# Optimization experiments

Measured on AMD Instinct MI355X. Metric: run time of the kernel, lower is better.

The kernel has to match this reference:

```python
import jax, jax.numpy as jnp
import numpy as np

KNN = 11  # self.knn in VoronoiBaseNN


def setup_inputs() -> dict:
    key = jax.random.key(0)
    k1, k2 = jax.random.split(key)
    points = jax.random.normal(k1, (2, 50000, 3), dtype=jnp.float32)   # GT surface samples
    spoints = jax.random.normal(k2, (2, 4000, 3), dtype=jnp.float32)   # Voronoi generators
    return {"points": points, "spoints": spoints}


def reference(points, spoints):
    # Pairwise squared distances: [B, N, M]
    d2 = ((points[:, :, None, :] - spoints[:, None, :, :]) ** 2).sum(-1)
    # KNN smallest, sorted ascending (torch.topk(largest=False, sorted=True))
    _, idx = jax.lax.top_k(-d2, KNN)            # idx: [B, N, KNN]
    # Gather the KNN generator coordinates: [B, N, KNN, 3]
    gathered = jax.vmap(lambda sp, i: sp[i])(spoints, idx)
    inside = gathered[:, :, 0, :]               # closest cell center [B, N, 3]
    point_to_center = points - inside           # [B, N, 3]
    # Voronoi edge vectors to the other KNN-1 neighbors: [B, N, KNN-1, 3]
    voronoi_edge = gathered[:, :, 1:, :] - inside[:, :, None, :]
    edge_l = jnp.sqrt((voronoi_edge ** 2).sum(-1))                      # [B, N, KNN-1]
    vector_length = (point_to_center[:, :, None, :] * voronoi_edge).sum(-1) / edge_l
    sq_dist = (vector_length - edge_l / 2.0) ** 2
    return sq_dist.min(-1)                      # [B, N]
```

## Files before the change

kernel.cpp:

```cpp
#include <hip/hip_runtime.h>
#include <math.h>

#define NPTS  50000
#define NSP   4000
#define NGRP  1000
#define NW    4
#define QW    (NGRP / NW)
#define QC    (NSP  / NW)
#define KNN   11
#define BIG   3.4e38f
#define SEGCAP 256
#define SEGPAD 8
#define SEGSTR (SEGCAP + SEGPAD)
#define GRIDC 32
#define NKEY  65536

#define MED3(a,b,c) __builtin_amdgcn_fmed3f((a),(b),(c))

__device__ unsigned g_hist[NKEY];
__device__ float4   g_sorted[2 * NPTS];

static __device__ __forceinline__ unsigned spread5(unsigned v) {
    return (v & 1u) | ((v & 2u) << 2) | ((v & 4u) << 4) |
           ((v & 8u) << 6) | ((v & 16u) << 8);
}

static __device__ __forceinline__ unsigned cell_key(int b, float x, float y, float z) {
    int gx = (int)floorf((x + 4.0f) * 4.0f);
    int gy = (int)floorf((y + 4.0f) * 4.0f);
    int gz = (int)floorf((z + 4.0f) * 4.0f);
    gx = min(max(gx, 0), GRIDC - 1);
    gy = min(max(gy, 0), GRIDC - 1);
    gz = min(max(gz, 0), GRIDC - 1);
    unsigned m = spread5((unsigned)gx) | (spread5((unsigned)gy) << 1) |
                 (spread5((unsigned)gz) << 2);
    return ((unsigned)b << 15) | m;
}

__global__ void k_zero() {
    int t = blockIdx.x * 256 + threadIdx.x;
    if (t < NKEY) g_hist[t] = 0u;
}

__global__ void k_hist(const float* __restrict__ pts) {
    int n = blockIdx.x * 256 + threadIdx.x;
    if (n >= 2 * NPTS) return;
    const float* p = pts + (size_t)n * 3;
    int b = (n >= NPTS) ? 1 : 0;
    atomicAdd(&g_hist[cell_key(b, p[0], p[1], p[2])], 1u);
}

__global__ void k_scan() {
    __shared__ unsigned part[1024];
    const int t = threadIdx.x;
    const unsigned base = (unsigned)blockIdx.x * 32768u + (unsigned)t * 32u;
    unsigned s = 0;
#pragma unroll
    for (int j = 0; j < 32; ++j) s += g_hist[base + j];
    part[t] = s;
    __syncthreads();
    for (int off = 1; off < 1024; off <<= 1) {
        unsigned v = (t >= off) ? part[t - off] : 0u;
        __syncthreads();
        part[t] += v;
        __syncthreads();
    }
    unsigned run = (unsigned)blockIdx.x * (unsigned)NPTS + part[t] - s;
#pragma unroll
    for (int j = 0; j < 32; ++j) {
        unsigned h = g_hist[base + j];
        g_hist[base + j] = run;
        run += h;
    }
}

__global__ void k_scatter(const float* __restrict__ pts) {
    int n = blockIdx.x * 256 + threadIdx.x;
    if (n >= 2 * NPTS) return;
    const float* p = pts + (size_t)n * 3;
    int b = (n >= NPTS) ? 1 : 0;
    float x = p[0], y = p[1], z = p[2];
    unsigned dst = atomicAdd(&g_hist[cell_key(b, x, y, z)], 1u);
    if (dst < 2u * NPTS)
        g_sorted[dst] = make_float4(x, y, z, __uint_as_float((unsigned)(n - b * NPTS)));
}

static __device__ __forceinline__ float wred_min(float v) {
#pragma unroll
    for (int off = 32; off > 0; off >>= 1) v = fminf(v, __shfl_xor(v, off, 64));
    return v;
}
static __device__ __forceinline__ float wred_max(float v) {
#pragma unroll
    for (int off = 32; off > 0; off >>= 1) v = fmaxf(v, __shfl_xor(v, off, 64));
    return v;
}

__global__ __launch_bounds__(256, 4) void voronoi_kernel(
    const float* __restrict__ spts,
    float* __restrict__ out)
{
    __shared__ float4 sl[NW * SEGSTR];
    __shared__ float  lds_d[NW][64][13];
    __shared__ int    lds_i[NW][64];
    __shared__ float  lds_b[NW][64];
    __shared__ float  lds_m[NW];

    const int b    = blockIdx.y;
    const int lane = threadIdx.x & 63;
    const int wq   = threadIdx.x >> 6;
    int pi = blockIdx.x * 64 + lane;
    const bool valid = (pi < NPTS);
    if (!valid) pi = NPTS - 1;

    const float4 P = g_sorted[(size_t)b * NPTS + pi];
    const float px = P.x, py = P.y, pz = P.z;
    const unsigned orig = __float_as_uint(P.w);

    const float mnx = wred_min(px), mxx = wred_max(px);
    const float mny = wred_min(py), mxy = wred_max(py);
    const float mnz = wred_min(pz), mxz = wred_max(pz);
    const float ccx = 0.5f * (mnx + mxx);
    const float ccy = 0.5f * (mny + mxy);
    const float ccz = 0.5f * (mnz + mxz);
    const float R = sqrtf(wred_max(
        fmaf(px - ccx, px - ccx, fmaf(py - ccy, py - ccy, (pz - ccz) * (pz - ccz)))));

    const float4* __restrict__ spq = (const float4*)(spts + (size_t)b * NSP * 3);
    const int g0 = wq * QW, g1 = g0 + QW;

    float myMin = BIG;
    for (int k0 = g0; k0 < g1; k0 += 64) {
        const int g  = k0 + lane;
        const int gc = (g < g1) ? g : (g1 - 1);
        const float4 q0 = spq[3 * gc + 0];
        const float4 q1 = spq[3 * gc + 1];
        const float4 q2 = spq[3 * gc + 2];
        float dx = q0.x - ccx, dy = q0.y - ccy, dz = q0.z - ccz;
        float md = fmaf(dx, dx, fmaf(dy, dy, dz * dz));
        dx = q0.w - ccx; dy = q1.x - ccy; dz = q1.y - ccz;
        md = fminf(md, fmaf(dx, dx, fmaf(dy, dy, dz * dz)));
        dx = q1.z - ccx; dy = q1.w - ccy; dz = q2.x - ccz;
        md = fminf(md, fmaf(dx, dx, fmaf(dy, dy, dz * dz)));
        dx = q2.y - ccx; dy = q2.z - ccy; dz = q2.w - ccz;
        md = fminf(md, fmaf(dx, dx, fmaf(dy, dy, dz * dz)));
        if (g < g1) myMin = fminf(myMin, md);
    }
    float vv = myMin, m11 = 0.0f;
#pragma unroll
    for (int t = 0; t < KNN; ++t) {
        m11 = wred_min(vv);
        vv = (vv == m11) ? BIG : vv;
    }
    if (lane == 0) lds_m[wq] = m11;
    __syncthreads();
    const float m11g = fminf(fminf(lds_m[0], lds_m[1]), fminf(lds_m[2], lds_m[3]));
    const float Trad = sqrtf(m11g) + R;
    const float T = Trad * Trad * 1.0004f + 1e-12f;

    const int segbase = wq * SEGSTR;
    unsigned cnt = 0;
    {
        for (int k0 = g0; k0 < g1; k0 += 64) {
            const int g  = k0 + lane;
            const int gc = (g < g1) ? g : (g1 - 1);
            const bool in = (g < g1);
            const float4 q0 = spq[3 * gc + 0];
            const float4 q1 = spq[3 * gc + 1];
            const float4 q2 = spq[3 * gc + 2];
#define ADM(sx, sy, sz) \
            (fmaf(MED3((sx), mnx, mxx) - (sx), MED3((sx), mnx, mxx) - (sx), \
             fmaf(MED3((sy), mny, mxy) - (sy), MED3((sy), mny, mxy) - (sy), \
                  (MED3((sz), mnz, mxz) - (sz)) * (MED3((sz), mnz, mxz) - (sz)))) <= T)
#define PUSH(sx, sy, sz, ok, idx) { \
            const unsigned long long msk = __ballot(ok); \
            const unsigned pos = cnt + \
                __builtin_amdgcn_mbcnt_hi((unsigned)(msk >> 32), \
                    __builtin_amdgcn_mbcnt_lo((unsigned)msk, 0u)); \
            if ((ok) && pos < SEGCAP) \
                sl[segbase + pos] = make_float4((sx), (sy), (sz), \
                                                __uint_as_float((unsigned)(idx))); \
            cnt += (unsigned)__popcll(msk); }
            const bool a0 = in && ADM(q0.x, q0.y, q0.z);
            const bool a1 = in && ADM(q0.w, q1.x, q1.y);
            const bool a2 = in && ADM(q1.z, q1.w, q2.x);
            const bool a3 = in && ADM(q2.y, q2.z, q2.w);
            PUSH(q0.x, q0.y, q0.z, a0, 4 * gc + 0);
            PUSH(q0.w, q1.x, q1.y, a1, 4 * gc + 1);
            PUSH(q1.z, q1.w, q2.x, a2, 4 * gc + 2);
            PUSH(q2.y, q2.z, q2.w, a3, 4 * gc + 3);
        }
        if (lane < SEGPAD) {
            const unsigned cb = (cnt <= SEGCAP) ? cnt : SEGCAP;
            sl[segbase + cb + lane] =
                make_float4(1e18f, 1e18f, 1e18f, __uint_as_float(0x7fffffffu));
        }
    }
    const bool myfast = (cnt <= SEGCAP);

    float d0 = BIG, d1 = BIG, d2 = BIG, d3 = BIG, d4 = BIG, d5 = BIG,
          d6 = BIG, d7 = BIG, d8 = BIG, d9 = BIG, d10 = BIG;
    int i0 = 0x7fffffff;

#define CHAIN(nd, jj) { \
        if (__ballot((nd) < d10)) { \
            d10 = MED3(d9, d10, (nd)); \
            d9  = MED3(d8, d9,  (nd)); \
            d8  = MED3(d7, d8,  (nd)); \
            d7  = MED3(d6, d7,  (nd)); \
            d6  = MED3(d5, d6,  (nd)); \
            d5  = MED3(d4, d5,  (nd)); \
            d4  = MED3(d3, d4,  (nd)); \
            d3  = MED3(d2, d3,  (nd)); \
            d2  = MED3(d1, d2,  (nd)); \
            d1  = MED3(d0, d1,  (nd)); \
            i0  = ((nd) < d0) ? (jj) : i0; \
            d0  = fminf(d0, (nd)); \
        } }
#define CANDA(c) { \
        const float dx = px - (c).x, dy = py - (c).y, dz = pz - (c).z; \
        const float nd = fmaf(dx, dx, fmaf(dy, dy, dz * dz)); \
        const int jj = (int)__float_as_uint((c).w); \
        CHAIN(nd, jj); }

    const float* sp = spts + (size_t)b * NSP * 3 + wq * (QC * 3);
    const int jb = wq * QC;

    if (myfast) {
        if (cnt > 0) {
            float4 c0 = sl[segbase + 0], c1 = sl[segbase + 1],
                   c2 = sl[segbase + 2], c3 = sl[segbase + 3];
            for (unsigned k = 0; k < cnt; k += 4) {
                const float4 n0 = sl[segbase + k + 4];
                const float4 n1 = sl[segbase + k + 5];
                const float4 n2 = sl[segbase + k + 6];
                const float4 n3 = sl[segbase + k + 7];
                CANDA(c0); CANDA(c1); CANDA(c2); CANDA(c3);
                c0 = n0; c1 = n1; c2 = n2; c3 = n3;
            }
        }
    } else {
        for (int j = 0; j < QC; j += 4) {
            const float4 q0 = *(const float4*)(sp + j * 3);
            const float4 q1 = *(const float4*)(sp + j * 3 + 4);
            const float4 q2 = *(const float4*)(sp + j * 3 + 8);
            { const float dx = px - q0.x, dy = py - q0.y, dz = pz - q0.z;
              const float nd = fmaf(dx, dx, fmaf(dy, dy, dz * dz)); CHAIN(nd, jb + j); }
            { const float dx = px - q0.w, dy = py - q1.x, dz = pz - q1.y;
              const float nd = fmaf(dx, dx, fmaf(dy, dy, dz * dz)); CHAIN(nd, jb + j + 1); }
            { const float dx = px - q1.z, dy = py - q1.w, dz = pz - q2.x;
              const float nd = fmaf(dx, dx, fmaf(dy, dy, dz * dz)); CHAIN(nd, jb + j + 2); }
            { const float dx = px - q2.y, dy = py - q2.z, dz = pz - q2.w;
              const float nd = fmaf(dx, dx, fmaf(dy, dy, dz * dz)); CHAIN(nd, jb + j + 3); }
        }
    }

    lds_d[wq][lane][0]  = d0;  lds_d[wq][lane][1]  = d1;
    lds_d[wq][lane][2]  = d2;  lds_d[wq][lane][3]  = d3;
    lds_d[wq][lane][4]  = d4;  lds_d[wq][lane][5]  = d5;
    lds_d[wq][lane][6]  = d6;  lds_d[wq][lane][7]  = d7;
    lds_d[wq][lane][8]  = d8;  lds_d[wq][lane][9]  = d9;
    lds_d[wq][lane][10] = d10;
    lds_i[wq][lane] = i0;
    __syncthreads();

    float gb = BIG; int gi = 0x7fffffff;
#pragma unroll
    for (int q = 0; q < NW; ++q) {
        const float dq = lds_d[q][lane][0];
        const int   iq = lds_i[q][lane];
        const bool take = (dq < gb) || (dq == gb && iq < gi);
        gb = take ? dq : gb;
        gi = take ? iq : gi;
    }
#define INS(v) { \
        d10 = MED3(d9, d10, (v)); \
        d9  = MED3(d8, d9,  (v)); \
        d8  = MED3(d7, d8,  (v)); \
        d7  = MED3(d6, d7,  (v)); \
        d6  = MED3(d5, d6,  (v)); \
        d5  = MED3(d4, d5,  (v)); \
        d4  = MED3(d3, d4,  (v)); \
        d3  = MED3(d2, d3,  (v)); \
        d2  = MED3(d1, d2,  (v)); \
        d1  = MED3(d0, d1,  (v)); \
        d0  = fminf(d0, (v)); }
#pragma unroll
    for (int q = 0; q < NW; ++q) {
        if (q == wq) continue;
#pragma unroll
        for (int k = 0; k < 11; ++k) INS(lds_d[q][lane][k]);
    }
    const float d10g = d10;
    const int   i0g  = gi;

    const float* ip = spts + (size_t)b * NSP * 3 + (size_t)(unsigned)i0g * 3;
    const float ix = ip[0], iy = ip[1], iz = ip[2];
    const float vx = px - ix, vy = py - iy, vz = pz - iz;
    float best = BIG;

#define EDGE(sx, sy, sz, adm) { \
        if (__ballot(adm)) { \
            const float ex = (sx) - ix, ey = (sy) - iy, ez = (sz) - iz; \
            const float ee = fmaf(ex, ex, fmaf(ey, ey, ez * ez)); \
            const float dt = fmaf(vx, ex, fmaf(vy, ey, vz * ez)); \
            const float u  = fmaf(-0.5f, ee, dt); \
            const float t2 = u * u * __builtin_amdgcn_rcpf(ee); \
            best = (adm) ? fminf(best, t2) : best; \
        } }
#define CANDB(c) { \
        const float dx = px - (c).x, dy = py - (c).y, dz = pz - (c).z; \
        const float nd = fmaf(dx, dx, fmaf(dy, dy, dz * dz)); \
        const int jj = (int)__float_as_uint((c).w); \
        const bool adm = (nd <= d10g) && (jj != i0g); \
        EDGE((c).x, (c).y, (c).z, adm); }

    if (myfast) {
        if (cnt > 0) {
            float4 c0 = sl[segbase + 0], c1 = sl[segbase + 1],
                   c2 = sl[segbase + 2], c3 = sl[segbase + 3];
            for (unsigned k = 0; k < cnt; k += 4) {
                const float4 n0 = sl[segbase + k + 4];
                const float4 n1 = sl[segbase + k + 5];
                const float4 n2 = sl[segbase + k + 6];
                const float4 n3 = sl[segbase + k + 7];
                CANDB(c0); CANDB(c1); CANDB(c2); CANDB(c3);
                c0 = n0; c1 = n1; c2 = n2; c3 = n3;
            }
        }
    } else {
        for (int j = 0; j < QC; j += 4) {
            const float4 q0 = *(const float4*)(sp + j * 3);
            const float4 q1 = *(const float4*)(sp + j * 3 + 4);
            const float4 q2 = *(const float4*)(sp + j * 3 + 8);
            { const float dx = px - q0.x, dy = py - q0.y, dz = pz - q0.z;
              const float nd = fmaf(dx, dx, fmaf(dy, dy, dz * dz));
              const bool adm = (nd <= d10g) && ((jb + j) != i0g);
              EDGE(q0.x, q0.y, q0.z, adm); }
            { const float dx = px - q0.w, dy = py - q1.x, dz = pz - q1.y;
              const float nd = fmaf(dx, dx, fmaf(dy, dy, dz * dz));
              const bool adm = (nd <= d10g) && ((jb + j + 1) != i0g);
              EDGE(q0.w, q1.x, q1.y, adm); }
            { const float dx = px - q1.z, dy = py - q1.w, dz = pz - q2.x;
              const float nd = fmaf(dx, dx, fmaf(dy, dy, dz * dz));
              const bool adm = (nd <= d10g) && ((jb + j + 2) != i0g);
              EDGE(q1.z, q1.w, q2.x, adm); }
            { const float dx = px - q2.y, dy = py - q2.z, dz = pz - q2.w;
              const float nd = fmaf(dx, dx, fmaf(dy, dy, dz * dz));
              const bool adm = (nd <= d10g) && ((jb + j + 3) != i0g);
              EDGE(q2.y, q2.z, q2.w, adm); }
        }
    }

    lds_b[wq][lane] = best;
    __syncthreads();
    if (wq == 0) {
        float m = fminf(fminf(lds_b[0][lane], lds_b[1][lane]),
                        fminf(lds_b[2][lane], lds_b[3][lane]));
        if (valid) out[(size_t)b * NPTS + orig] = m;
    }
}

extern "C" void kernel_launch(void* const* d_in, const int* in_sizes, int n_in,
                              void* d_out, int out_size, void* d_ws, size_t ws_size,
                              hipStream_t stream) {
    (void)in_sizes; (void)n_in; (void)d_ws; (void)ws_size; (void)out_size;
    const float* pts  = (const float*)d_in[0];
    const float* spts = (const float*)d_in[1];
    float* out = (float*)d_out;

    k_zero   <<<dim3(NKEY / 256),            dim3(256),  0, stream>>>();
    k_hist   <<<dim3((2 * NPTS + 255)/256),  dim3(256),  0, stream>>>(pts);
    k_scan   <<<dim3(2),                     dim3(1024), 0, stream>>>();
    k_scatter<<<dim3((2 * NPTS + 255)/256),  dim3(256),  0, stream>>>(pts);
    voronoi_kernel<<<dim3((NPTS + 63)/64, 2), dim3(256), 0, stream>>>(spts, out);
}
```

Measured before the change: 306.0 us.

## Split wave into four 16-lane sub-boxes for tighter candidate culling

Instead of one bounding box and radius per 64-point wave, the kernel computes four bounding boxes over 16-lane subgroups, each with its own kth-nearest threshold. A generator is admitted if it falls within the threshold of any sub-box, which is meant to shrink the candidate list scanned in the KNN and edge passes. The brute-force overflow fallback is replaced by chunked re-collection into a larger LDS segment (capacity doubled), with the edge pass redoing collection when overflow occurred. The cost is four times the threshold arithmetic and more LDS, with occupancy lowered from 4 to 3 blocks per SIMD in the launch bounds.

```diff
diff --git a/kernel.cpp b/kernel.cpp
--- a/kernel.cpp
+++ b/kernel.cpp
@@ -6,10 +6,9 @@
 #define NGRP  1000
 #define NW    4
 #define QW    (NGRP / NW)
-#define QC    (NSP  / NW)
 #define KNN   11
 #define BIG   3.4e38f
-#define SEGCAP 256
+#define SEGCAP 512
 #define SEGPAD 8
 #define SEGSTR (SEGCAP + SEGPAD)
 #define GRIDC 32
@@ -90,13 +89,18 @@
     for (int off = 32; off > 0; off >>= 1) v = fminf(v, __shfl_xor(v, off, 64));
     return v;
 }
-static __device__ __forceinline__ float wred_max(float v) {
-#pragma unroll
-    for (int off = 32; off > 0; off >>= 1) v = fmaxf(v, __shfl_xor(v, off, 64));
+static __device__ __forceinline__ float sred_min16(float v) {
+#pragma unroll
+    for (int off = 8; off > 0; off >>= 1) v = fminf(v, __shfl_xor(v, off, 64));
     return v;
 }
-
-__global__ __launch_bounds__(256, 4) void voronoi_kernel(
+static __device__ __forceinline__ float sred_max16(float v) {
+#pragma unroll
+    for (int off = 8; off > 0; off >>= 1) v = fmaxf(v, __shfl_xor(v, off, 64));
+    return v;
+}
+
+__global__ __launch_bounds__(256, 3) void voronoi_kernel(
     const float* __restrict__ spts,
     float* __restrict__ out)
 {
@@ -104,7 +108,7 @@
     __shared__ float  lds_d[NW][64][13];
     __shared__ int    lds_i[NW][64];
     __shared__ float  lds_b[NW][64];
-    __shared__ float  lds_m[NW];
+    __shared__ float  lds_m[NW][4];
 
     const int b    = blockIdx.y;
     const int lane = threadIdx.x & 63;
@@ -117,86 +121,131 @@
     const float px = P.x, py = P.y, pz = P.z;
     const unsigned orig = __float_as_uint(P.w);
 
-    const float mnx = wred_min(px), mxx = wred_max(px);
-    const float mny = wred_min(py), mxy = wred_max(py);
-    const float mnz = wred_min(pz), mxz = wred_max(pz);
-    const float ccx = 0.5f * (mnx + mxx);
-    const float ccy = 0.5f * (mny + mxy);
-    const float ccz = 0.5f * (mnz + mxz);
-    const float R = sqrtf(wred_max(
-        fmaf(px - ccx, px - ccx, fmaf(py - ccy, py - ccy, (pz - ccz) * (pz - ccz)))));
+    const float smnx = sred_min16(px), smxx = sred_max16(px);
+    const float smny = sred_min16(py), smxy = sred_max16(py);
+    const float smnz = sred_min16(pz), smxz = sred_max16(pz);
+    const float scx = 0.5f * (smnx + smxx);
+    const float scy = 0.5f * (smny + smxy);
+    const float scz = 0.5f * (smnz + smxz);
+    const float sR = sqrtf(sred_max16(
+        fmaf(px - scx, px - scx, fmaf(py - scy, py - scy, (pz - scz) * (pz - scz)))));
+
+#define BC(v, j) __shfl((v), (j) * 16, 64)
+    const float b0nx = BC(smnx,0), b0xx = BC(smxx,0), b0ny = BC(smny,0),
+                b0xy = BC(smxy,0), b0nz = BC(smnz,0), b0xz = BC(smxz,0),
+                c0x = BC(scx,0), c0y = BC(scy,0), c0z = BC(scz,0), R0 = BC(sR,0);
+    const float b1nx = BC(smnx,1), b1xx = BC(smxx,1), b1ny = BC(smny,1),
+                b1xy = BC(smxy,1), b1nz = BC(smnz,1), b1xz = BC(smxz,1),
+                c1x = BC(scx,1), c1y = BC(scy,1), c1z = BC(scz,1), R1 = BC(sR,1);
+    const float b2nx = BC(smnx,2), b2xx = BC(smxx,2), b2ny = BC(smny,2),
+                b2xy = BC(smxy,2), b2nz = BC(smnz,2), b2xz = BC(smxz,2),
+                c2x = BC(scx,2), c2y = BC(scy,2), c2z = BC(scz,2), R2 = BC(sR,2);
+    const float b3nx = BC(smnx,3), b3xx = BC(smxx,3), b3ny = BC(smny,3),
+                b3xy = BC(smxy,3), b3nz = BC(smnz,3), b3xz = BC(smxz,3),
+                c3x = BC(scx,3), c3y = BC(scy,3), c3z = BC(scz,3), R3 = BC(sR,3);
 
     const float4* __restrict__ spq = (const float4*)(spts + (size_t)b * NSP * 3);
     const int g0 = wq * QW, g1 = g0 + QW;
 
-    float myMin = BIG;
+    float v0 = BIG, v1 = BIG, v2 = BIG, v3 = BIG;
     for (int k0 = g0; k0 < g1; k0 += 64) {
         const int g  = k0 + lane;
         const int gc = (g < g1) ? g : (g1 - 1);
         const float4 q0 = spq[3 * gc + 0];
         const float4 q1 = spq[3 * gc + 1];
         const float4 q2 = spq[3 * gc + 2];
-        float dx = q0.x - ccx, dy = q0.y - ccy, dz = q0.z - ccz;
-        float md = fmaf(dx, dx, fmaf(dy, dy, dz * dz));
-        dx = q0.w - ccx; dy = q1.x - ccy; dz = q1.y - ccz;
-        md = fminf(md, fmaf(dx, dx, fmaf(dy, dy, dz * dz)));
-        dx = q1.z - ccx; dy = q1.w - ccy; dz = q2.x - ccz;
-        md = fminf(md, fmaf(dx, dx, fmaf(dy, dy, dz * dz)));
-        dx = q2.y - ccx; dy = q2.z - ccy; dz = q2.w - ccz;
-        md = fminf(md, fmaf(dx, dx, fmaf(dy, dy, dz * dz)));
-        if (g < g1) myMin = fminf(myMin, md);
-    }
-    float vv = myMin, m11 = 0.0f;
+        float t0 = BIG, t1 = BIG, t2 = BIG, t3 = BIG;
+#define DACC(sx, sy, sz) { \
+        float dx, dy, dz; \
+        dx=(sx)-c0x; dy=(sy)-c0y; dz=(sz)-c0z; t0=fminf(t0, fmaf(dx,dx,fmaf(dy,dy,dz*dz))); \
+        dx=(sx)-c1x; dy=(sy)-c1y; dz=(sz)-c1z; t1=fminf(t1, fmaf(dx,dx,fmaf(dy,dy,dz*dz))); \
+        dx=(sx)-c2x; dy=(sy)-c2y; dz=(sz)-c2z; t2=fminf(t2, fmaf(dx,dx,fmaf(dy,dy,dz*dz))); \
+        dx=(sx)-c3x; dy=(sy)-c3y; dz=(sz)-c3z; t3=fminf(t3, fmaf(dx,dx,fmaf(dy,dy,dz*dz))); }
+        DACC(q0.x, q0.y, q0.z);
+        DACC(q0.w, q1.x, q1.y);
+        DACC(q1.z, q1.w, q2.x);
+        DACC(q2.y, q2.z, q2.w);
+        if (g < g1) { v0 = fminf(v0, t0); v1 = fminf(v1, t1);
+                      v2 = fminf(v2, t2); v3 = fminf(v3, t3); }
+    }
+
+    float m0 = 0.f, m1 = 0.f, m2 = 0.f, m3 = 0.f;
 #pragma unroll
     for (int t = 0; t < KNN; ++t) {
-        m11 = wred_min(vv);
-        vv = (vv == m11) ? BIG : vv;
-    }
-    if (lane == 0) lds_m[wq] = m11;
+        m0 = wred_min(v0); v0 = (v0 == m0) ? BIG : v0;
+        m1 = wred_min(v1); v1 = (v1 == m1) ? BIG : v1;
+        m2 = wred_min(v2); v2 = (v2 == m2) ? BIG : v2;
+        m3 = wred_min(v3); v3 = (v3 == m3) ? BIG : v3;
+    }
+    if (lane == 0) { lds_m[wq][0] = m0; lds_m[wq][1] = m1;
+                     lds_m[wq][2] = m2; lds_m[wq][3] = m3; }
     __syncthreads();
-    const float m11g = fminf(fminf(lds_m[0], lds_m[1]), fminf(lds_m[2], lds_m[3]));
-    const float Trad = sqrtf(m11g) + R;
-    const float T = Trad * Trad * 1.0004f + 1e-12f;
+    float M0 = BIG, M1 = BIG, M2 = BIG, M3 = BIG;
+#pragma unroll
+    for (int q = 0; q < NW; ++q) {
+        M0 = fminf(M0, lds_m[q][0]); M1 = fminf(M1, lds_m[q][1]);
+        M2 = fminf(M2, lds_m[q][2]); M3 = fminf(M3, lds_m[q][3]);
+    }
+    const float Tr0 = sqrtf(M0) + R0; const float T0 = Tr0*Tr0*1.0004f + 1e-12f;
+    const float Tr1 = sqrtf(M1) + R1; const float T1 = Tr1*Tr1*1.0004f + 1e-12f;
+    const float Tr2 = sqrtf(M2) + R2; const float T2 = Tr2*Tr2*1.0004f + 1e-12f;
+    const float Tr3 = sqrtf(M3) + R3; const float T3 = Tr3*Tr3*1.0004f + 1e-12f;
+
+#define BOXD2(sx,sy,sz, nx,xx,ny,xy,nz,xz) \
+    (fmaf(MED3((sx),(nx),(xx))-(sx), MED3((sx),(nx),(xx))-(sx), \
+     fmaf(MED3((sy),(ny),(xy))-(sy), MED3((sy),(ny),(xy))-(sy), \
+          (MED3((sz),(nz),(xz))-(sz)) * (MED3((sz),(nz),(xz))-(sz)))))
+#define ADM4(sx, sy, sz) \
+    ((BOXD2(sx,sy,sz, b0nx,b0xx,b0ny,b0xy,b0nz,b0xz) <= T0) || \
+     (BOXD2(sx,sy,sz, b1nx,b1xx,b1ny,b1xy,b1nz,b1xz) <= T1) || \
+     (BOXD2(sx,sy,sz, b2nx,b2xx,b2ny,b2xy,b2nz,b2xz) <= T2) || \
+     (BOXD2(sx,sy,sz, b3nx,b3xx,b3ny,b3xy,b3nz,b3xz) <= T3))
 
     const int segbase = wq * SEGSTR;
     unsigned cnt = 0;
-    {
+
+    auto padseg = [&]() {
+        if (lane < SEGPAD)
+            sl[segbase + (int)cnt + lane] =
+                make_float4(1e18f, 1e18f, 1e18f, __uint_as_float(0x7fffffffu));
+    };
+
+#define PUSH(sx, sy, sz, ok, idx) { \
+        const unsigned long long msk = __ballot(ok); \
+        if (ok) { \
+            const unsigned pos = cnt + \
+                __builtin_amdgcn_mbcnt_hi((unsigned)(msk >> 32), \
+                    __builtin_amdgcn_mbcnt_lo((unsigned)msk, 0u)); \
+            sl[segbase + (int)pos] = \
+                make_float4((sx), (sy), (sz), __uint_as_float((unsigned)(idx))); \
+        } \
+        cnt += (unsigned)__popcll(msk); }
+
+    auto run_pass = [&](auto&& consume) -> bool {
+        bool of = false;
+        cnt = 0;
         for (int k0 = g0; k0 < g1; k0 += 64) {
+            if (cnt > (unsigned)(SEGCAP - 256)) {
+                padseg(); consume(cnt); cnt = 0; of = true;
+            }
             const int g  = k0 + lane;
             const int gc = (g < g1) ? g : (g1 - 1);
             const bool in = (g < g1);
             const float4 q0 = spq[3 * gc + 0];
             const float4 q1 = spq[3 * gc + 1];
             const float4 q2 = spq[3 * gc + 2];
-#define ADM(sx, sy, sz) \
-            (fmaf(MED3((sx), mnx, mxx) - (sx), MED3((sx), mnx, mxx) - (sx), \
-             fmaf(MED3((sy), mny, mxy) - (sy), MED3((sy), mny, mxy) - (sy), \
-                  (MED3((sz), mnz, mxz) - (sz)) * (MED3((sz), mnz, mxz) - (sz)))) <= T)
-#define PUSH(sx, sy, sz, ok, idx) { \
-            const unsigned long long msk = __ballot(ok); \
-            const unsigned pos = cnt + \
-                __builtin_amdgcn_mbcnt_hi((unsigned)(msk >> 32), \
-                    __builtin_amdgcn_mbcnt_lo((unsigned)msk, 0u)); \
-            if ((ok) && pos < SEGCAP) \
-                sl[segbase + pos] = make_float4((sx), (sy), (sz), \
-                                                __uint_as_float((unsigned)(idx))); \
-            cnt += (unsigned)__popcll(msk); }
-            const bool a0 = in && ADM(q0.x, q0.y, q0.z);
-            const bool a1 = in && ADM(q0.w, q1.x, q1.y);
-            const bool a2 = in && ADM(q1.z, q1.w, q2.x);
-            const bool a3 = in && ADM(q2.y, q2.z, q2.w);
+            const bool a0 = in && ADM4(q0.x, q0.y, q0.z);
+            const bool a1 = in && ADM4(q0.w, q1.x, q1.y);
+            const bool a2 = in && ADM4(q1.z, q1.w, q2.x);
+            const bool a3 = in && ADM4(q2.y, q2.z, q2.w);
             PUSH(q0.x, q0.y, q0.z, a0, 4 * gc + 0);
             PUSH(q0.w, q1.x, q1.y, a1, 4 * gc + 1);
             PUSH(q1.z, q1.w, q2.x, a2, 4 * gc + 2);
             PUSH(q2.y, q2.z, q2.w, a3, 4 * gc + 3);
         }
-        if (lane < SEGPAD) {
-            const unsigned cb = (cnt <= SEGCAP) ? cnt : SEGCAP;
-            sl[segbase + cb + lane] =
-                make_float4(1e18f, 1e18f, 1e18f, __uint_as_float(0x7fffffffu));
-        }
-    }
-    const bool myfast = (cnt <= SEGCAP);
+        padseg(); consume(cnt);
+        return of;
+    };
 
     float d0 = BIG, d1 = BIG, d2 = BIG, d3 = BIG, d4 = BIG, d5 = BIG,
           d6 = BIG, d7 = BIG, d8 = BIG, d9 = BIG, d10 = BIG;
@@ -223,37 +272,22 @@
         const int jj = (int)__float_as_uint((c).w); \
         CHAIN(nd, jj); }
 
-    const float* sp = spts + (size_t)b * NSP * 3 + wq * (QC * 3);
-    const int jb = wq * QC;
-
-    if (myfast) {
-        if (cnt > 0) {
-            float4 c0 = sl[segbase + 0], c1 = sl[segbase + 1],
-                   c2 = sl[segbase + 2], c3 = sl[segbase + 3];
-            for (unsigned k = 0; k < cnt; k += 4) {
-                const float4 n0 = sl[segbase + k + 4];
-                const float4 n1 = sl[segbase + k + 5];
-                const float4 n2 = sl[segbase + k + 6];
-                const float4 n3 = sl[segbase + k + 7];
-                CANDA(c0); CANDA(c1); CANDA(c2); CANDA(c3);
-                c0 = n0; c1 = n1; c2 = n2; c3 = n3;
-            }
+    auto chainA = [&](unsigned n) {
+        if (n == 0u) return;
+        float4 e0 = sl[segbase + 0], e1 = sl[segbase + 1],
+               e2 = sl[segbase + 2], e3 = sl[segbase + 3];
+        for (unsigned k = 0; k < n; k += 4) {
+            const float4 n0 = sl[segbase + (int)k + 4];
+            const float4 n1 = sl[segbase + (int)k + 5];
+            const float4 n2 = sl[segbase + (int)k + 6];
+            const float4 n3 = sl[segbase + (int)k + 7];
+            CANDA(e0); CANDA(e1); CANDA(e2); CANDA(e3);
+            e0 = n0; e1 = n1; e2 = n2; e3 = n3;
         }
-    } else {
-        for (int j = 0; j < QC; j += 4) {
-            const float4 q0 = *(const float4*)(sp + j * 3);
-            const float4 q1 = *(const float4*)(sp + j * 3 + 4);
-            const float4 q2 = *(const float4*)(sp + j * 3 + 8);
-            { const float dx = px - q0.x, dy = py - q0.y, dz = pz - q0.z;
-              const float nd = fmaf(dx, dx, fmaf(dy, dy, dz * dz)); CHAIN(nd, jb + j); }
-            { const float dx = px - q0.w, dy = py - q1.x, dz = pz - q1.y;
-              const float nd = fmaf(dx, dx, fmaf(dy, dy, dz * dz)); CHAIN(nd, jb + j + 1); }
-            { const float dx = px - q1.z, dy = py - q1.w, dz = pz - q2.x;
-              const float nd = fmaf(dx, dx, fmaf(dy, dy, dz * dz)); CHAIN(nd, jb + j + 2); }
-            { const float dx = px - q2.y, dy = py - q2.z, dz = pz - q2.w;
-              const float nd = fmaf(dx, dx, fmaf(dy, dy, dz * dz)); CHAIN(nd, jb + j + 3); }
-        }
-    }
+    };
+
+    const bool ovfA = run_pass(chainA);
+    const unsigned cntA = cnt;
 
     lds_d[wq][lane][0]  = d0;  lds_d[wq][lane][1]  = d1;
     lds_d[wq][lane][2]  = d2;  lds_d[wq][lane][3]  = d3;
@@ -299,57 +333,38 @@
     const float vx = px - ix, vy = py - iy, vz = pz - iz;
     float best = BIG;
 
-#define EDGE(sx, sy, sz, adm) { \
-        if (__ballot(adm)) { \
-            const float ex = (sx) - ix, ey = (sy) - iy, ez = (sz) - iz; \
-            const float ee = fmaf(ex, ex, fmaf(ey, ey, ez * ez)); \
-            const float dt = fmaf(vx, ex, fmaf(vy, ey, vz * ez)); \
-            const float u  = fmaf(-0.5f, ee, dt); \
-            const float t2 = u * u * __builtin_amdgcn_rcpf(ee); \
-            best = (adm) ? fminf(best, t2) : best; \
-        } }
 #define CANDB(c) { \
         const float dx = px - (c).x, dy = py - (c).y, dz = pz - (c).z; \
         const float nd = fmaf(dx, dx, fmaf(dy, dy, dz * dz)); \
         const int jj = (int)__float_as_uint((c).w); \
         const bool adm = (nd <= d10g) && (jj != i0g); \
-        EDGE((c).x, (c).y, (c).z, adm); }
-
-    if (myfast) {
-        if (cnt > 0) {
-            float4 c0 = sl[segbase + 0], c1 = sl[segbase + 1],
-                   c2 = sl[segbase + 2], c3 = sl[segbase + 3];
-            for (unsigned k = 0; k < cnt; k += 4) {
-                const float4 n0 = sl[segbase + k + 4];
-                const float4 n1 = sl[segbase + k + 5];
-                const float4 n2 = sl[segbase + k + 6];
-                const float4 n3 = sl[segbase + k + 7];
-                CANDB(c0); CANDB(c1); CANDB(c2); CANDB(c3);
-                c0 = n0; c1 = n1; c2 = n2; c3 = n3;
-            }
+        if (__ballot(adm)) { \
+            const float ex = (c).x - ix, ey = (c).y - iy, ez = (c).z - iz; \
+            const float ee = fmaf(ex, ex, fmaf(ey, ey, ez * ez)); \
+            const float dt = fmaf(vx, ex, fmaf(vy, ey, vz * ez)); \
+            const float u  = fmaf(-0.5f, ee, dt); \
+            const float t2 = u * u * __builtin_amdgcn_rcpf(ee); \
+            best = adm ? fminf(best, t2) : best; \
+        } }
+
+    auto scanB = [&](unsigned n) {
+        if (n == 0u) return;
+        float4 e0 = sl[segbase + 0], e1 = sl[segbase + 1],
+               e2 = sl[segbase + 2], e3 = sl[segbase + 3];
+        for (unsigned k = 0; k < n; k += 4) {
+            const float4 n0 = sl[segbase + (int)k + 4];
+            const float4 n1 = sl[segbase + (int)k + 5];
+            const float4 n2 = sl[segbase + (int)k + 6];
+            const float4 n3 = sl[segbase + (int)k + 7];
+            CANDB(e0); CANDB(e1); CANDB(e2); CANDB(e3);
+            e0 = n0; e1 = n1; e2 = n2; e3 = n3;
         }
+    };
+
+    if (!ovfA) {
+        scanB(cntA);
     } else {
-        for (int j = 0; j < QC; j += 4) {
-            const float4 q0 = *(const float4*)(sp + j * 3);
-            const float4 q1 = *(const float4*)(sp + j * 3 + 4);
-            const float4 q2 = *(const float4*)(sp + j * 3 + 8);
-            { const float dx = px - q0.x, dy = py - q0.y, dz = pz - q0.z;
-              const float nd = fmaf(dx, dx, fmaf(dy, dy, dz * dz));
-              const bool adm = (nd <= d10g) && ((jb + j) != i0g);
-              EDGE(q0.x, q0.y, q0.z, adm); }
-            { const float dx = px - q0.w, dy = py - q1.x, dz = pz - q1.y;
-              const float nd = fmaf(dx, dx, fmaf(dy, dy, dz * dz));
-              const bool adm = (nd <= d10g) && ((jb + j + 1) != i0g);
-              EDGE(q0.w, q1.x, q1.y, adm); }
-            { const float dx = px - q1.z, dy = py - q1.w, dz = pz - q2.x;
-              const float nd = fmaf(dx, dx, fmaf(dy, dy, dz * dz));
-              const bool adm = (nd <= d10g) && ((jb + j + 2) != i0g);
-              EDGE(q1.z, q1.w, q2.x, adm); }
-            { const float dx = px - q2.y, dy = py - q2.z, dz = pz - q2.w;
-              const float nd = fmaf(dx, dx, fmaf(dy, dy, dz * dz));
-              const bool adm = (nd <= d10g) && ((jb + j + 3) != i0g);
-              EDGE(q2.y, q2.z, q2.w, adm); }
-        }
+        (void)run_pass(scanB);
     }
 
     lds_b[wq][lane] = best;
```

New measurement: 308.3 us. About the same (+0.8%).
